# Kernel tuning notes

Measured on AMD Instinct MI355X. Metric: run time of the kernel, lower is better.

The kernel has to match this reference:

```python
import jax, jax.numpy as jnp
import numpy as np

B, D, T = 16, 256, 4096          # batch, latent_d, latent_t
NQ, K, DC = 8, 1024, 128          # num RVQ layers, codebook size, codebook dim
SAMPLE_IDX = (0, 1, 2, 3)         # deterministic stand-in for weighted np.random.choice


def setup_inputs() -> dict:
    key = jax.random.key(0)
    ks = jax.random.split(key, 6)
    return {
        "diffusion_starts": jax.random.normal(ks[0], (B, D, T), jnp.float32),
        "target_latent_codes": jax.random.randint(ks[1], (B, NQ, T), 0, K),
        "Win": jax.random.normal(ks[2], (NQ, DC, D), jnp.float32) / np.float32(np.sqrt(D)),
        "b_in": jnp.zeros((NQ, DC), jnp.float32),
        "Wout": jax.random.normal(ks[3], (NQ, D, DC), jnp.float32) / np.float32(np.sqrt(DC)),
        "b_out": jnp.zeros((NQ, D), jnp.float32),
        "embed": jax.random.normal(ks[4], (NQ, K, DC), jnp.float32),
    }


def reference(diffusion_starts, target_latent_codes, Win, b_in, Wout, b_out, embed):
    residuals = diffusion_starts  # [B, D, T]
    losses = []
    for i in range(NQ):
        x = residuals.transpose(0, 2, 1)                 # [B, T, D]
        xp = jnp.einsum('btd,cd->btc', x, Win[i]) + b_in[i]   # project_in -> [B, T, DC]
        # Codebook is fully detached in the torch module (quantize path detached,
        # logits path detached), so stop_gradient once here.
        e = jax.lax.stop_gradient(embed[i])              # [K, DC]
        x2 = jnp.sum(xp * xp, axis=-1, keepdims=True)    # [B, T, 1]
        e2 = jnp.sum(e * e, axis=-1)                     # [K]
        sq = x2 - 2.0 * jnp.einsum('btc,kc->btk', xp, e) + e2  # [B, T, K] sum_d (x-e)^2
        ind = jnp.argmin(sq, axis=-1)                    # nearest-neighbor lookup
        quant = e[ind]                                   # [B, T, DC]
        qout = jnp.einsum('btc,dc->btd', quant, Wout[i]) + b_out[i]  # project_out
        residuals = residuals - jax.lax.stop_gradient(qout.transpose(0, 2, 1))
        if i in SAMPLE_IDX:
            logits = -sq / DC                            # mean over latent_d of (x - c)^2, negated
            tgt = target_latent_codes[:, i, :]           # [B, T]
            lse = jax.nn.logsumexp(logits, axis=-1)      # [B, T]
            picked = jnp.take_along_axis(logits, tgt[..., None], axis=-1)[..., 0]
            losses.append(jnp.mean(lse - picked))        # cross_entropy, reduction='mean'
    return jnp.mean(jnp.stack(losses))
```

## Files before the change

### kernel.cpp

```cpp
#include <hip/hip_runtime.h>
#include <math.h>

#define B_   16
#define D_   256
#define T_   4096
#define NQn  8
#define K_   1024
#define DC_  128
#define M_   65536

typedef short bf16x8 __attribute__((ext_vector_type(8)));
typedef float f32x4  __attribute__((ext_vector_type(4)));

static __device__ __forceinline__ unsigned short f2bf(float f) {
    unsigned u = __float_as_uint(f);
    unsigned r = (u + 0x7fffu + ((u >> 16) & 1u)) >> 16;
    return (unsigned short)r;
}

static __device__ __forceinline__ int pk2(float lo, float hi) {
    int r;
    asm("v_cvt_pk_bf16_f32 %0, %1, %2" : "=v"(r) : "v"(lo), "v"(hi));
    return r;
}
static __device__ __forceinline__ int sub2(int x, int t) {
    float xl = __uint_as_float(((unsigned)x) << 16);
    float xh = __uint_as_float(((unsigned)x) & 0xFFFF0000u);
    float tl = __uint_as_float(((unsigned)t) << 16);
    float th = __uint_as_float(((unsigned)t) & 0xFFFF0000u);
    return pk2(xl - tl, xh - th);
}

static __device__ __forceinline__ f32x4 MFMA(bf16x8 a, bf16x8 b, f32x4 c) {
    return __builtin_amdgcn_mfma_f32_16x16x32_bf16(a, b, c, 0, 0, 0);
}

#define EXP2(x) __builtin_amdgcn_exp2f(x)
#define LOG2(x) __builtin_amdgcn_logf(x)

__global__ void zero_acc_k(float* acc) { acc[0] = 0.f; }
__global__ void final_k(const float* __restrict__ acc, float* __restrict__ out) {
    out[0] = acc[0] * (1.f / 262144.f);
}

__global__ __launch_bounds__(256) void reformat_k(
    const float* __restrict__ Win, const float* __restrict__ bin,
    const float* __restrict__ emb, unsigned short* __restrict__ stream,
    float* __restrict__ gbias)
{
    const int bid = blockIdx.x;
    const int tid = threadIdx.x;
    if (bid == 320) {
        gbias[4096 + tid]       = bin[tid];
        gbias[4096 + 256 + tid] = bin[256 + tid];
        return;
    }
    int u = bid * 256 + tid;
    int idx = u >> 10;
    int q = idx / 20, r = idx - q * 20;
    int w = u & 1023;
    int lane = w & 63, blk = w >> 6;
    int l15 = lane & 15, lg4 = lane >> 4;
    unsigned short o[8];
    if (r < 4) {
        int c  = 32 * r + 16 * (blk >> 3) + l15;
        int d0 = 32 * (blk & 7) + 8 * lg4;
        const float* s = Win + ((size_t)q * DC_ + c) * D_ + d0;
        #pragma unroll
        for (int j = 0; j < 8; ++j) o[j] = f2bf(s[j]);
    } else {
        int ch = r - 4;
        int code = (ch * 4 + (blk >> 2)) * 16 + l15;
        int s4 = blk & 3;
        const float* s = emb + ((size_t)q * K_ + code) * DC_ + 32 * s4 + 4 * lg4;
        const float ESC = 1.44269504089f / 64.0f;
        #pragma unroll
        for (int j = 0; j < 8; ++j)
            o[j] = f2bf(s[16 * (j >> 2) + (j & 3)] * ESC);
    }
    *(int4*)&stream[(size_t)u * 8] = *(int4*)o;
}

__global__ __launch_bounds__(256) void prep_tab_k(
    const float* __restrict__ Wout, const float* __restrict__ bout,
    const float* __restrict__ emb,
    unsigned short* __restrict__ tab, float* __restrict__ gbias)
{
    __shared__ float E[16][128];
    const int iq = blockIdx.x >> 6;
    const int k0 = (blockIdx.x & 63) << 4;
    const int tid = threadIdx.x;
    {
        const float* src = emb + ((size_t)iq * K_ + k0) * DC_;
        #pragma unroll
        for (int it = 0; it < 2; ++it) {
            int lin = it * 1024 + tid * 4;
            float4 v = *(const float4*)(src + lin);
            *(float4*)&E[lin >> 7][lin & 127] = v;
        }
    }
    __syncthreads();
    if (tid < 16) {
        float e2 = 0.f;
        for (int c2 = 0; c2 < 128; ++c2) { float e = E[tid][c2]; e2 += e * e; }
        gbias[iq * K_ + k0 + tid] = e2 * (1.44269504089f / 128.f);
    }
    if (iq < 3) {
        const int d = tid;
        float acc[16];
        #pragma unroll
        for (int kk = 0; kk < 16; ++kk) acc[kk] = 0.f;
        const float* wp = Wout + ((size_t)iq * D_ + d) * DC_;
        for (int c2 = 0; c2 < 128; ++c2) {
            float w = wp[c2];
            #pragma unroll
            for (int kk = 0; kk < 16; ++kk) acc[kk] = fmaf(E[kk][c2], w, acc[kk]);
        }
        float bo = bout[iq * D_ + d];
        unsigned short* tq = tab + ((size_t)iq << 18);
        #pragma unroll
        for (int kk = 0; kk < 16; ++kk)
            tq[((size_t)(k0 + kk) << 8) + d] = f2bf(acc[kk] + bo);
    }
}

#define GLDS(SRC, DST) __builtin_amdgcn_global_load_lds( \
    (const __attribute__((address_space(1))) unsigned int*)(SRC), \
    (__attribute__((address_space(3))) unsigned int*)(DST), 16, 0, 0)

#define ITERTOP(BUFP) do { \
    BUFP = LDSM + (cslot << 14); \
    asm volatile("s_waitcnt vmcnt(4)" ::: "memory"); \
    __builtin_amdgcn_s_barrier(); \
    int ss_ = (cslot == 0) ? 2 : cslot - 1; \
    const char* sc_ = sp + (wv << 12) + (lane << 4); \
    char* dc_ = LDSM + (ss_ << 14) + (wv << 12); \
    GLDS(sc_, dc_); GLDS(sc_ + 1024, dc_ + 1024); \
    GLDS(sc_ + 2048, dc_ + 2048); GLDS(sc_ + 3072, dc_ + 3072); \
    sp += 16384; if (sp == send) sp = sbase; \
    cslot = (cslot == 2) ? 0 : cslot + 1; \
    __builtin_amdgcn_sched_barrier(0); \
} while (0)

static __device__ __forceinline__ void mfma_chunk(
    const char* bufp, int lane, const bf16x8 (&xpf)[2][4], f32x4 (&acc)[8])
{
    #pragma unroll
    for (int cfp = 0; cfp < 2; ++cfp)
        #pragma unroll
        for (int cl = 0; cl < 2; ++cl) {
            f32x4 a0 = {0.f, 0.f, 0.f, 0.f}, a1 = a0;
            #pragma unroll
            for (int ss = 0; ss < 4; ++ss) {
                bf16x8 a = *(const bf16x8*)(bufp + ((((cfp * 2 + cl) * 4 + ss) * 64 + lane) << 4));
                a0 = MFMA(a, xpf[0][ss], a0);
                a1 = MFMA(a, xpf[1][ss], a1);
            }
            acc[cfp * 4 + cl * 2 + 0] = a0;
            acc[cfp * 4 + cl * 2 + 1] = a1;
        }
}

template<bool LEAN>
static __device__ __forceinline__ void epi8(
    const f32x4 (&acc)[8], int ch, const float* gq, int lg4,
    const int (&tgt)[2], float (&lsum)[2], float (&bv)[2], int (&bi)[2],
    float (&pick)[2])
{
    #pragma unroll
    for (int cfp = 0; cfp < 2; ++cfp)
        #pragma unroll
        for (int cl = 0; cl < 2; ++cl) {
            int cfg = ch * 4 + cfp * 2 + cl;
            float4 gv = *(const float4*)(gq + cfg * 16 + lg4 * 4);
            int cbb = cfg * 16 + lg4 * 4;
            #pragma unroll
            for (int rf = 0; rf < 2; ++rf) {
                const f32x4& A = acc[cfp * 4 + cl * 2 + rf];
                float l0 = A[0] - gv.x, l1 = A[1] - gv.y;
                float l2 = A[2] - gv.z, l3 = A[3] - gv.w;
                lsum[rf] += (EXP2(l0) + EXP2(l1)) + (EXP2(l2) + EXP2(l3));
                if (!LEAN) {
                    float m01 = fmaxf(l0, l1), m23 = fmaxf(l2, l3);
                    float lm = fmaxf(m01, m23);
                    int jl = (m23 > m01) ? ((l3 > l2) ? 3 : 2) : ((l1 > l0) ? 1 : 0);
                    if (lm > bv[rf]) { bv[rf] = lm; bi[rf] = cbb + jl; }
                }
                if ((tgt[rf] >> 2) == (cbb >> 2)) {
                    int myj = tgt[rf] & 3;
                    pick[rf] = (myj & 2) ? ((myj & 1) ? l3 : l2) : ((myj & 1) ? l1 : l0);
                }
            }
        }
}

template<bool LEAN>
static __device__ __forceinline__ void q_body(
    int q, char* LDSM, const float* gb,
    const char*& sp, const char* sbase, const char* send, int& cslot,
    int wv, int lane, int l15, int lg4,
    bf16x8 (&xb)[2][8], const unsigned short* tab, float& loss)
{
    int tgt[2];
    {
        const int* tl = (const int*)(LDSM + 67584);
        tgt[0] = tl[(wv * 4 + q) * 32 + l15];
        tgt[1] = tl[(wv * 4 + q) * 32 + 16 + l15];
    }

    bf16x8 xpf[2][4];
    #pragma unroll
    for (int S = 0; S < 4; ++S) {
        const char* bufp;
        ITERTOP(bufp);
        f32x4 a00 = {0.f, 0.f, 0.f, 0.f}, a01 = a00, a10 = a00, a11 = a00;
        #pragma unroll
        for (int ss = 0; ss < 8; ++ss) {
            bf16x8 w0 = *(const bf16x8*)(bufp + (((ss) * 64 + lane) << 4));
            bf16x8 w1 = *(const bf16x8*)(bufp + (((8 + ss) * 64 + lane) << 4));
            a00 = MFMA(w0, xb[0][ss], a00);
            a01 = MFMA(w0, xb[1][ss], a01);
            a10 = MFMA(w1, xb[0][ss], a10);
            a11 = MFMA(w1, xb[1][ss], a11);
        }
        float4 b0 = *(const float4*)(gb + 4096 + q * 128 + 32 * S + 4 * lg4);
        float4 b1 = *(const float4*)(gb + 4096 + q * 128 + 32 * S + 16 + 4 * lg4);
        int4 u0, u1;
        u0.x = pk2(a00[0] + b0.x, a00[1] + b0.y);
        u0.y = pk2(a00[2] + b0.z, a00[3] + b0.w);
        u0.z = pk2(a10[0] + b1.x, a10[1] + b1.y);
        u0.w = pk2(a10[2] + b1.z, a10[3] + b1.w);
        xpf[0][S] = *(bf16x8*)&u0;
        u1.x = pk2(a01[0] + b0.x, a01[1] + b0.y);
        u1.y = pk2(a01[2] + b0.z, a01[3] + b0.w);
        u1.z = pk2(a11[0] + b1.x, a11[1] + b1.y);
        u1.w = pk2(a11[2] + b1.z, a11[3] + b1.w);
        xpf[1][S] = *(bf16x8*)&u1;
    }

    const float* gq = gb + (q << 10);
    float lsum[2] = {0.f, 0.f};
    float bv[2]   = {-1e30f, -1e30f};
    int   bi[2]   = {0, 0};
    float pick[2] = {0.f, 0.f};
    f32x4 A[8], Bq[8];
    {
        const char* bufp;
        ITERTOP(bufp);
        mfma_chunk(bufp, lane, xpf, A);
    }
    #pragma unroll 1
    for (int t = 0; t < 7; ++t) {
        {
            const char* bufp;
            ITERTOP(bufp);
            mfma_chunk(bufp, lane, xpf, Bq);
            epi8<LEAN>(A, 2 * t, gq, lg4, tgt, lsum, bv, bi, pick);
        }
        {
            const char* bufp;
            ITERTOP(bufp);
            mfma_chunk(bufp, lane, xpf, A);
            epi8<LEAN>(Bq, 2 * t + 1, gq, lg4, tgt, lsum, bv, bi, pick);
        }
    }
    {
        const char* bufp;
        ITERTOP(bufp);
        mfma_chunk(bufp, lane, xpf, Bq);
        epi8<LEAN>(A, 14, gq, lg4, tgt, lsum, bv, bi, pick);
    }
    epi8<LEAN>(Bq, 15, gq, lg4, tgt, lsum, bv, bi, pick);

    #pragma unroll
    for (int rf = 0; rf < 2; ++rf) {
        #pragma unroll
        for (int off = 16; off <= 32; off <<= 1) {
            lsum[rf] += __shfl_xor(lsum[rf], off);
            pick[rf] += __shfl_xor(pick[rf], off);
            if (!LEAN) {
                float om = __shfl_xor(bv[rf], off);
                int   ob = __shfl_xor(bi[rf], off);
                if (om > bv[rf] || (om == bv[rf] && ob < bi[rf])) { bv[rf] = om; bi[rf] = ob; }
            }
        }
        if (lane < 16) loss += LOG2(lsum[rf]) - pick[rf];
    }

    if (!LEAN) {
        const unsigned short* tq = tab + ((size_t)q << 18);
        #pragma unroll
        for (int rf = 0; rf < 2; ++rf) {
            const unsigned short* trow = tq + ((size_t)bi[rf] << 8) + (lg4 << 3);
            #pragma unroll
            for (int s = 0; s < 8; ++s) {
                int4 tv = *(const int4*)(trow + (s << 5));
                int4 xv = *(int4*)&xb[rf][s];
                int4 ov;
                ov.x = sub2(xv.x, tv.x); ov.y = sub2(xv.y, tv.y);
                ov.z = sub2(xv.z, tv.z); ov.w = sub2(xv.w, tv.w);
                *(int4*)&xb[rf][s] = ov;
            }
        }
    }
}

__global__ __launch_bounds__(256, 2) void rvq_k(
    const float* __restrict__ X,
    const unsigned short* __restrict__ stream,
    const float* __restrict__ gbias,
    const unsigned short* __restrict__ tab,
    const int* __restrict__ tlc,
    float* __restrict__ accp)
{
    __shared__ __align__(16) char LDSM[69632];

    const int tid  = threadIdx.x;
    const int lane = tid & 63;
    const int wv   = tid >> 6;
    const int l15  = lane & 15;
    const int lg4  = lane >> 4;
    const int row_base = blockIdx.x * 128 + wv * 32;

    bf16x8 xb[2][8];
    #pragma unroll
    for (int rf = 0; rf < 2; ++rf) {
        const int row = row_base + rf * 16 + l15;
        const float* xpr = X + ((size_t)(row >> 12) << 20) + (row & (T_ - 1));
        #pragma unroll
        for (int s = 0; s < 8; ++s) {
            float f[8];
            #pragma unroll
            for (int j = 0; j < 8; ++j)
                f[j] = xpr[(size_t)((s << 5) + (lg4 << 3) + j) << 12];
            int4 u;
            u.x = pk2(f[0], f[1]); u.y = pk2(f[2], f[3]);
            u.z = pk2(f[4], f[5]); u.w = pk2(f[6], f[7]);
            xb[rf][s] = *(bf16x8*)&u;
        }
    }

    {
        int* tl = (int*)(LDSM + 67584);
        int q0 = lg4;
        int r0 = row_base + l15, r1 = row_base + 16 + l15;
        int t0 = tlc[(size_t)(r0 >> 12) * (NQn * T_) + q0 * T_ + (r0 & (T_ - 1))];
        int t1 = tlc[(size_t)(r1 >> 12) * (NQn * T_) + q0 * T_ + (r1 & (T_ - 1))];
        tl[(wv * 4 + q0) * 32 + l15] = t0;
        tl[(wv * 4 + q0) * 32 + 16 + l15] = t1;
    }
    __builtin_amdgcn_sched_barrier(0);

    const char* sbase = (const char*)stream;
    const char* send  = sbase + 80 * 16384;
    {
        const char* gs = (const char*)gbias;
        #pragma unroll
        for (int k = 0; k < 4; ++k)
            GLDS(gs + (((k * 4 + wv) * 64 + lane) << 4),
                 LDSM + 49152 + ((k * 4 + wv) << 10));
        if (wv < 2)
            GLDS(gs + 16384 + ((wv * 64 + lane) << 4),
                 LDSM + 49152 + 16384 + (wv << 10));
    }
    {
        const char* s0 = sbase + (wv << 12) + (lane << 4);
        char* d0 = LDSM + (wv << 12);
        GLDS(s0, d0); GLDS(s0 + 1024, d0 + 1024);
        GLDS(s0 + 2048, d0 + 2048); GLDS(s0 + 3072, d0 + 3072);
        const char* s1 = s0 + 16384;
        char* d1 = d0 + 16384;
        GLDS(s1, d1); GLDS(s1 + 1024, d1 + 1024);
        GLDS(s1 + 2048, d1 + 2048); GLDS(s1 + 3072, d1 + 3072);
    }
    const char* sp = sbase + 32768;
    int cslot = 0;
    __syncthreads();

    float loss = 0.f;
    const float* gb = (const float*)(LDSM + 49152);

    #pragma unroll 1
    for (int q = 0; q < 3; ++q)
        q_body<false>(q, LDSM, gb, sp, sbase, send, cslot,
                      wv, lane, l15, lg4, xb, tab, loss);
    q_body<true>(3, LDSM, gb, sp, sbase, send, cslot,
                 wv, lane, l15, lg4, xb, tab, loss);

    asm volatile("s_waitcnt vmcnt(0)" ::: "memory");
    #pragma unroll
    for (int off = 1; off < 64; off <<= 1) loss += __shfl_xor(loss, off);
    if (lane == 0) atomicAdd(accp, loss * 0.69314718056f);
}

extern "C" void kernel_launch(void* const* d_in, const int* in_sizes, int n_in,
                              void* d_out, int out_size, void* d_ws, size_t ws_size,
                              hipStream_t stream_)
{
    (void)in_sizes; (void)n_in; (void)out_size; (void)ws_size;
    const float* dstart = (const float*)d_in[0];
    const int*   tlc    = (const int*)d_in[1];
    const float* Win    = (const float*)d_in[2];
    const float* bin    = (const float*)d_in[3];
    const float* Wout   = (const float*)d_in[4];
    const float* bout   = (const float*)d_in[5];
    const float* emb    = (const float*)d_in[6];

    char* ws = (char*)d_ws;
    size_t off = 0;
    unsigned short* strm = (unsigned short*)(ws + off); off += (size_t)80 * 16384;
    unsigned short* tab  = (unsigned short*)(ws + off); off += (size_t)3 * K_ * D_ * 2;
    float*          gbias= (float*)(ws + off);          off += (size_t)4608 * 4;
    float*          accp = (float*)(ws + off);          off += 256;

    zero_acc_k<<<1, 1, 0, stream_>>>(accp);
    reformat_k<<<321, 256, 0, stream_>>>(Win, bin, emb, strm, gbias);
    prep_tab_k<<<256, 256, 0, stream_>>>(Wout, bout, emb, tab, gbias);
    rvq_k<<<512, 256, 0, stream_>>>(dstart, strm, gbias, tab, tlc, accp);
    final_k<<<1, 1, 0, stream_>>>(accp, (float*)d_out);
}
```

Baseline: 168.8 us.

## Pack argmax index into exp mantissa bits and recompute target logit via MFMA

The per-element argmin tracking and target-pick selection in the softmax epilogue are removed. The codebook index is now stored in the low mantissa bits of each exp value, so one fmaxf per group tracks the argmax and lsum uses those packed values. The target logit is recomputed after the loop with a few extra MFMAs against the target codebook row read from the staged buffer. This cuts VALU work in the hot epilogue, but it perturbs exp values and the logsumexp slightly, and ties and near-ties may resolve to a different index than a true argmin.

Measured after the change: 159.6 us. 5.5% less time.

```diff
diff --git a/kernel.cpp b/kernel.cpp
--- a/kernel.cpp
+++ b/kernel.cpp
@@ -164,8 +164,7 @@
 template<bool LEAN>
 static __device__ __forceinline__ void epi8(
     const f32x4 (&acc)[8], int ch, const float* gq, int lg4,
-    const int (&tgt)[2], float (&lsum)[2], float (&bv)[2], int (&bi)[2],
-    float (&pick)[2])
+    float (&lsum)[2], float (&bv)[2])
 {
     #pragma unroll
     for (int cfp = 0; cfp < 2; ++cfp)
@@ -173,22 +172,23 @@
         for (int cl = 0; cl < 2; ++cl) {
             int cfg = ch * 4 + cfp * 2 + cl;
             float4 gv = *(const float4*)(gq + cfg * 16 + lg4 * 4);
-            int cbb = cfg * 16 + lg4 * 4;
             #pragma unroll
             for (int rf = 0; rf < 2; ++rf) {
                 const f32x4& A = acc[cfp * 4 + cl * 2 + rf];
-                float l0 = A[0] - gv.x, l1 = A[1] - gv.y;
-                float l2 = A[2] - gv.z, l3 = A[3] - gv.w;
-                lsum[rf] += (EXP2(l0) + EXP2(l1)) + (EXP2(l2) + EXP2(l3));
-                if (!LEAN) {
-                    float m01 = fmaxf(l0, l1), m23 = fmaxf(l2, l3);
-                    float lm = fmaxf(m01, m23);
-                    int jl = (m23 > m01) ? ((l3 > l2) ? 3 : 2) : ((l1 > l0) ? 1 : 0);
-                    if (lm > bv[rf]) { bv[rf] = lm; bi[rf] = cbb + jl; }
-                }
-                if ((tgt[rf] >> 2) == (cbb >> 2)) {
-                    int myj = tgt[rf] & 3;
-                    pick[rf] = (myj & 2) ? ((myj & 1) ? l3 : l2) : ((myj & 1) ? l1 : l0);
+                float e0 = EXP2(A[0] - gv.x);
+                float e1 = EXP2(A[1] - gv.y);
+                float e2 = EXP2(A[2] - gv.z);
+                float e3 = EXP2(A[3] - gv.w);
+                if (LEAN) {
+                    lsum[rf] += (e0 + e1) + (e2 + e3);
+                } else {
+                    unsigned cv = (unsigned)cfg;
+                    float p0 = __uint_as_float((__float_as_uint(e0) & 0xFFFFFF00u) | cv);
+                    float p1 = __uint_as_float(((__float_as_uint(e1) & 0xFFFFFF00u) | cv) | 64u);
+                    float p2 = __uint_as_float(((__float_as_uint(e2) & 0xFFFFFF00u) | cv) | 128u);
+                    float p3 = __uint_as_float(((__float_as_uint(e3) & 0xFFFFFF00u) | cv) | 192u);
+                    lsum[rf] += (p0 + p1) + (p2 + p3);
+                    bv[rf] = fmaxf(bv[rf], fmaxf(fmaxf(p0, p1), fmaxf(p2, p3)));
                 }
             }
         }
@@ -199,7 +199,7 @@
     int q, char* LDSM, const float* gb,
     const char*& sp, const char* sbase, const char* send, int& cslot,
     int wv, int lane, int l15, int lg4,
-    bf16x8 (&xb)[2][8], const unsigned short* tab, float& loss)
+    bf16x8 (&xb)[2][8], const unsigned short* tab, const char* sq, float& loss)
 {
     int tgt[2];
     {
@@ -240,9 +240,8 @@
 
     const float* gq = gb + (q << 10);
     float lsum[2] = {0.f, 0.f};
-    float bv[2]   = {-1e30f, -1e30f};
+    float bv[2]   = {0.f, 0.f};
     int   bi[2]   = {0, 0};
-    float pick[2] = {0.f, 0.f};
     f32x4 A[8], Bq[8];
     {
         const char* bufp;
@@ -255,36 +254,60 @@
             const char* bufp;
             ITERTOP(bufp);
             mfma_chunk(bufp, lane, xpf, Bq);
-            epi8<LEAN>(A, 2 * t, gq, lg4, tgt, lsum, bv, bi, pick);
+            epi8<LEAN>(A, 2 * t, gq, lg4, lsum, bv);
         }
         {
             const char* bufp;
             ITERTOP(bufp);
             mfma_chunk(bufp, lane, xpf, A);
-            epi8<LEAN>(Bq, 2 * t + 1, gq, lg4, tgt, lsum, bv, bi, pick);
+            epi8<LEAN>(Bq, 2 * t + 1, gq, lg4, lsum, bv);
         }
     }
     {
         const char* bufp;
         ITERTOP(bufp);
         mfma_chunk(bufp, lane, xpf, Bq);
-        epi8<LEAN>(A, 14, gq, lg4, tgt, lsum, bv, bi, pick);
-    }
-    epi8<LEAN>(Bq, 15, gq, lg4, tgt, lsum, bv, bi, pick);
-
+        epi8<LEAN>(A, 14, gq, lg4, lsum, bv);
+    }
+    epi8<LEAN>(Bq, 15, gq, lg4, lsum, bv);
+
+    float pickv[2];
     #pragma unroll
     for (int rf = 0; rf < 2; ++rf) {
+        int t = tgt[rf];
+        const char* fb = sq + ((4 + (t >> 6)) << 14)
+                       + (((((t >> 4) & 3) << 8) + (lg4 << 4) + (t & 15)) << 4);
+        bf16x8 f0 = *(const bf16x8*)(fb);
+        bf16x8 f1 = *(const bf16x8*)(fb + 1024);
+        bf16x8 f2 = *(const bf16x8*)(fb + 2048);
+        bf16x8 f3 = *(const bf16x8*)(fb + 3072);
+        f32x4 pa = {0.f, 0.f, 0.f, 0.f};
+        pa = MFMA(f0, xpf[rf][0], pa);
+        pa = MFMA(f1, xpf[rf][1], pa);
+        pa = MFMA(f2, xpf[rf][2], pa);
+        pa = MFMA(f3, xpf[rf][3], pa);
+        int r = l15 & 3;
+        float dv = (r == 0) ? pa[0] : ((r == 1) ? pa[1] : ((r == 2) ? pa[2] : pa[3]));
+        float gt = gq[t];
+        pickv[rf] = (lg4 == (l15 >> 2)) ? (dv - gt) : 0.f;
+    }
+
+    #pragma unroll
+    for (int rf = 0; rf < 2; ++rf) {
+        float pk10 = 0.f;
+        if (!LEAN) {
+            unsigned pb = __float_as_uint(bv[rf]);
+            unsigned code = ((pb & 63u) << 4) | (unsigned)(lg4 << 2) | ((pb >> 6) & 3u);
+            pk10 = __uint_as_float((pb & 0xFFFFFC00u) | code);
+        }
         #pragma unroll
         for (int off = 16; off <= 32; off <<= 1) {
-            lsum[rf] += __shfl_xor(lsum[rf], off);
-            pick[rf] += __shfl_xor(pick[rf], off);
-            if (!LEAN) {
-                float om = __shfl_xor(bv[rf], off);
-                int   ob = __shfl_xor(bi[rf], off);
-                if (om > bv[rf] || (om == bv[rf] && ob < bi[rf])) { bv[rf] = om; bi[rf] = ob; }
-            }
-        }
-        if (lane < 16) loss += LOG2(lsum[rf]) - pick[rf];
+            lsum[rf]  += __shfl_xor(lsum[rf], off);
+            pickv[rf] += __shfl_xor(pickv[rf], off);
+            if (!LEAN) pk10 = fmaxf(pk10, __shfl_xor(pk10, off));
+        }
+        if (!LEAN) bi[rf] = (int)(__float_as_uint(pk10) & 1023u);
+        if (lane < 16) loss += LOG2(lsum[rf]) - pickv[rf];
     }
 
     if (!LEAN) {
@@ -383,9 +406,11 @@
     #pragma unroll 1
     for (int q = 0; q < 3; ++q)
         q_body<false>(q, LDSM, gb, sp, sbase, send, cslot,
-                      wv, lane, l15, lg4, xb, tab, loss);
+                      wv, lane, l15, lg4, xb, tab,
+                      sbase + (size_t)q * 327680, loss);
     q_body<true>(3, LDSM, gb, sp, sbase, send, cslot,
-                 wv, lane, l15, lg4, xb, tab, loss);
+                 wv, lane, l15, lg4, xb, tab,
+                 sbase + (size_t)3 * 327680, loss);
 
     asm volatile("s_waitcnt vmcnt(0)" ::: "memory");
     #pragma unroll
```
